# Kernel optimization log

Hardware: AMD Instinct MI355X
Metric: run time of the kernel (lower is better)

The kernel has to match this reference:

```python
import jax, jax.numpy as jnp
import numpy as np

N, E, F_IN, H, D, HID, G = 50000, 800000, 64, 4, 32, 128, 1024
NEG_SLOPE = 0.2


def setup_inputs():
    key = jax.random.key(0)
    ks = jax.random.split(key, 32)
    inp = {
        "x": jax.random.normal(ks[0], (N, F_IN), dtype=jnp.float32),
        "edge_index": jax.random.randint(ks[1], (2, E), 0, N, dtype=jnp.int64),
        "batch": jnp.sort(jax.random.randint(ks[2], (N,), 0, G, dtype=jnp.int64)),
    }
    dims = [F_IN, HID, HID]
    i = 3
    for l, din in enumerate(dims):
        s = 1.0 / np.sqrt(din)
        inp[f"Wl{l}"] = jax.random.normal(ks[i], (din, H * D), dtype=jnp.float32) * s; i += 1
        inp[f"bl{l}"] = jnp.zeros((H * D,), dtype=jnp.float32)
        inp[f"Wr{l}"] = jax.random.normal(ks[i], (din, H * D), dtype=jnp.float32) * s; i += 1
        inp[f"br{l}"] = jnp.zeros((H * D,), dtype=jnp.float32)
        inp[f"att{l}"] = jax.random.normal(ks[i], (H, D), dtype=jnp.float32) * (1.0 / np.sqrt(D)); i += 1
        inp[f"b{l}"] = jnp.zeros((H * D,), dtype=jnp.float32)
    inp["Wh"] = jax.random.normal(ks[i], (HID, 1), dtype=jnp.float32) * (1.0 / np.sqrt(HID))
    inp["bh"] = jnp.zeros((1,), dtype=jnp.float32)
    return inp


def gatv2_layer(x, src, dst, Wl, bl, Wr, br, att, b):
    # GATv2Conv (eval mode, no dropout): e_ij = att . leaky_relu(Wl x_j + Wr x_i)
    xl = (x @ Wl + bl).reshape(-1, H, D)   # source transform
    xr = (x @ Wr + br).reshape(-1, H, D)   # target transform
    m = xl[src] + xr[dst]                  # [E,H,D]
    e = jnp.where(m >= 0, m, NEG_SLOPE * m)
    score = jnp.einsum("ehd,hd->eh", e, att)          # [E,H]
    smax = jax.ops.segment_max(score, dst, num_segments=N)  # [N,H]
    expv = jnp.exp(score - smax[dst])
    denom = jax.ops.segment_sum(expv, dst, num_segments=N)
    alpha = expv / denom[dst]                          # softmax over in-edges of dst
    agg = jax.ops.segment_sum(alpha[:, :, None] * xl[src], dst, num_segments=N)
    return agg.reshape(-1, H * D) + b


def reference(x, edge_index, batch, Wl0, bl0, Wr0, br0, att0, b0,
              Wl1, bl1, Wr1, br1, att1, b1,
              Wl2, bl2, Wr2, br2, att2, b2, Wh, bh):
    src, dst = edge_index[0], edge_index[1]
    params = [(Wl0, bl0, Wr0, br0, att0, b0),
              (Wl1, bl1, Wr1, br1, att1, b1),
              (Wl2, bl2, Wr2, br2, att2, b2)]
    h = x
    for p in params:
        h = gatv2_layer(h, src, dst, *p)
        h = jax.nn.elu(h)  # dropout inactive in eval
    # global mean pool over graphs
    sums = jax.ops.segment_sum(h, batch, num_segments=G)
    cnt = jax.ops.segment_sum(jnp.ones((h.shape[0],), h.dtype), batch, num_segments=G)
    pooled = sums / jnp.maximum(cnt, 1.0)[:, None]
    return pooled @ Wh + bh
```

## Files before the change

kernel.cpp:

```cpp
#include <hip/hip_runtime.h>
#include <math.h>

#define N_NODES 50000
#define N_EDGES 800000
#define HD 128
#define GG 1024
#define NEG_SLOPE 0.2f
#define SCAN_B 1024
#define NB ((N_NODES + SCAN_B - 1) / SCAN_B)

typedef __attribute__((ext_vector_type(8))) short bf16x8;
typedef __attribute__((ext_vector_type(4))) float f32x4;

__device__ __forceinline__ unsigned short f2bf(float v) {
    unsigned u = __float_as_uint(v);
    u += 0x7fff + ((u >> 16) & 1);
    return (unsigned short)(u >> 16);
}
__device__ __forceinline__ float bf2f(unsigned short s) {
    return __uint_as_float((unsigned)s << 16);
}

__global__ void convert_x(const float* __restrict__ x, unsigned short* __restrict__ Xh,
                          unsigned short* __restrict__ Xl, int total)
{
    int i = blockIdx.x * 256 + threadIdx.x;
    if (i >= total) return;
    float v = x[i];
    unsigned short hi = f2bf(v);
    unsigned short lo = f2bf(v - bf2f(hi));
    Xh[i] = hi; Xl[i] = lo;
}

__global__ void convert_w(const float* __restrict__ Wl, const float* __restrict__ Wr,
                          unsigned short* __restrict__ Wth, unsigned short* __restrict__ Wtl,
                          int K)
{
    int t = blockIdx.x * 256 + threadIdx.x;
    if (t >= 256 * K) return;
    int c = t / K, k = t - c * K;
    float v = (c < 128) ? Wl[(size_t)k * 128 + c] : Wr[(size_t)k * 128 + (c - 128)];
    unsigned short hi = f2bf(v);
    unsigned short lo = f2bf(v - bf2f(hi));
    Wth[t] = hi; Wtl[t] = lo;
}

template<int K>
__launch_bounds__(256)
__global__ void gemm_mfma(const unsigned short* __restrict__ Xh, const unsigned short* __restrict__ Xl,
                          const unsigned short* __restrict__ Wth, const unsigned short* __restrict__ Wtl,
                          const float* __restrict__ bl, const float* __restrict__ br,
                          float* __restrict__ Cl, float* __restrict__ Cr, int n)
{
    constexpr int KC = 32;
    constexpr int NCH = K / KC;
    constexpr int XR = 40;
    __shared__ unsigned short XsH[64 * XR], XsL[64 * XR];
    __shared__ unsigned short WsH[256 * XR], WsL[256 * XR];
    const int tid  = threadIdx.x;
    const int wave = tid >> 6;
    const int lane = tid & 63;
    const int quad = lane >> 4;
    const int l15  = lane & 15;
    const int row0 = blockIdx.x * 64;

    f32x4 acc[4][4];
    #pragma unroll
    for (int i = 0; i < 4; i++)
        #pragma unroll
        for (int j = 0; j < 4; j++) acc[i][j] = (f32x4){0.f, 0.f, 0.f, 0.f};

    for (int ch = 0; ch < NCH; ch++) {
        const int k0 = ch * KC;
        {
            const int r = tid >> 2, seg = tid & 3;
            const int row = row0 + r;
            const size_t go = (size_t)row * K + k0 + seg * 8;
            uint4 vh = make_uint4(0, 0, 0, 0), vl = make_uint4(0, 0, 0, 0);
            if (row < n) { vh = *(const uint4*)(Xh + go); vl = *(const uint4*)(Xl + go); }
            *(uint4*)&XsH[r * XR + seg * 8] = vh;
            *(uint4*)&XsL[r * XR + seg * 8] = vl;
        }
        #pragma unroll
        for (int i = 0; i < 4; i++) {
            const int f = tid + i * 256;
            const int wr = f >> 2, seg = f & 3;
            const size_t go = (size_t)wr * K + k0 + seg * 8;
            *(uint4*)&WsH[wr * XR + seg * 8] = *(const uint4*)(Wth + go);
            *(uint4*)&WsL[wr * XR + seg * 8] = *(const uint4*)(Wtl + go);
        }
        __syncthreads();

        bf16x8 ah[4], al[4];
        #pragma unroll
        for (int mt = 0; mt < 4; mt++) {
            ah[mt] = *(const bf16x8*)&XsH[(mt * 16 + l15) * XR + quad * 8];
            al[mt] = *(const bf16x8*)&XsL[(mt * 16 + l15) * XR + quad * 8];
        }
        #pragma unroll
        for (int nt = 0; nt < 4; nt++) {
            const int wr = wave * 64 + nt * 16 + l15;
            const bf16x8 bh = *(const bf16x8*)&WsH[wr * XR + quad * 8];
            const bf16x8 bo = *(const bf16x8*)&WsL[wr * XR + quad * 8];
            #pragma unroll
            for (int mt = 0; mt < 4; mt++) {
                acc[mt][nt] = __builtin_amdgcn_mfma_f32_16x16x32_bf16(ah[mt], bh, acc[mt][nt], 0, 0, 0);
                acc[mt][nt] = __builtin_amdgcn_mfma_f32_16x16x32_bf16(ah[mt], bo, acc[mt][nt], 0, 0, 0);
                acc[mt][nt] = __builtin_amdgcn_mfma_f32_16x16x32_bf16(al[mt], bh, acc[mt][nt], 0, 0, 0);
            }
        }
        __syncthreads();
    }

    const bool isL = (wave < 2);
    const int colbase = (wave & 1) * 64;
    const float* bias = isL ? bl : br;
    float* C = isL ? Cl : Cr;
    #pragma unroll
    for (int nt = 0; nt < 4; nt++) {
        const float bv = bias[colbase + nt * 16 + l15];
        #pragma unroll
        for (int mt = 0; mt < 4; mt++) {
            #pragma unroll
            for (int r = 0; r < 4; r++) {
                const int row = row0 + mt * 16 + quad * 4 + r;
                if (row < n)
                    C[(size_t)row * 128 + colbase + nt * 16 + l15] = acc[mt][nt][r] + bv;
            }
        }
    }
}

__global__ void deg_hist(const int* __restrict__ dst, int* __restrict__ deg) {
    int e = blockIdx.x * 256 + threadIdx.x;
    if (e < N_EDGES) atomicAdd(&deg[dst[e]], 1);
}

__launch_bounds__(SCAN_B)
__global__ void scan_block(const int* __restrict__ deg, int* __restrict__ rowptr,
                           int* __restrict__ btot)
{
    __shared__ int s[SCAN_B];
    const int tid = threadIdx.x;
    const int i = blockIdx.x * SCAN_B + tid;
    int v = (i < N_NODES) ? deg[i] : 0;
    s[tid] = v;
    __syncthreads();
    for (int off = 1; off < SCAN_B; off <<= 1) {
        int t = (tid >= off) ? s[tid - off] : 0;
        __syncthreads();
        s[tid] += t;
        __syncthreads();
    }
    if (i < N_NODES) rowptr[i] = s[tid] - v;
    if (tid == SCAN_B - 1) btot[blockIdx.x] = s[SCAN_B - 1];
}

__global__ void scan_btot(const int* __restrict__ btot, int* __restrict__ boff) {
    if (threadIdx.x == 0) {
        int a = 0;
        for (int b = 0; b < NB; b++) { boff[b] = a; a += btot[b]; }
        boff[NB] = a;
    }
}

__global__ void scan_add(const int* __restrict__ boff, int* __restrict__ rowptr,
                         int* __restrict__ cursor)
{
    int i = blockIdx.x * 256 + threadIdx.x;
    if (i < N_NODES) {
        int r = rowptr[i] + boff[i >> 10];
        rowptr[i] = r;
        cursor[i] = r;
    }
    if (i == N_NODES) rowptr[N_NODES] = boff[NB];
}

__global__ void scatter_csr(const int* __restrict__ src, const int* __restrict__ dst,
                            int* __restrict__ cursor, int* __restrict__ csr_src)
{
    int e = blockIdx.x * 256 + threadIdx.x;
    if (e >= N_EDGES) return;
    int pos = atomicAdd(&cursor[dst[e]], 1);
    csr_src[pos] = src[e];
}

__global__ void build_gptr(const int* __restrict__ batch, int* __restrict__ gptr) {
    int i = blockIdx.x * 256 + threadIdx.x;
    if (i > N_NODES) return;
    if (i == 0) {
        for (int g = 0; g <= batch[0]; g++) gptr[g] = 0;
    } else if (i == N_NODES) {
        for (int g = batch[N_NODES - 1] + 1; g <= GG; g++) gptr[g] = N_NODES;
    } else {
        int b0 = batch[i - 1], b1 = batch[i];
        for (int g = b0 + 1; g <= b1; g++) gptr[g] = i;
    }
}

__launch_bounds__(256)
__global__ void node_attn(const float* __restrict__ xl, const float* __restrict__ xr,
                          const int* __restrict__ rowptr, const int* __restrict__ csr_src,
                          const float* __restrict__ att, const float* __restrict__ bvec,
                          unsigned short* __restrict__ Hh, unsigned short* __restrict__ Hl)
{
    const int node = (blockIdx.x * 256 + threadIdx.x) >> 6;
    const int lane = threadIdx.x & 63;
    if (node >= N_NODES) return;
    const int grp = lane >> 4;
    const int li  = lane & 15;

    const size_t nb = (size_t)node * HD + li * 8;
    const float4 xr0 = *(const float4*)(xr + nb);
    const float4 xr1 = *(const float4*)(xr + nb + 4);
    const float4 aw0 = *(const float4*)(att + li * 8);
    const float4 aw1 = *(const float4*)(att + li * 8 + 4);
    const int beg = rowptr[node];
    const int end = rowptr[node + 1];

    float m = -1e30f, l = 0.f;
    float4 a0 = make_float4(0.f, 0.f, 0.f, 0.f);
    float4 a1 = make_float4(0.f, 0.f, 0.f, 0.f);

    int e0 = beg + grp;
    int s0 = (e0 < end) ? csr_src[e0] : 0;
    float4 v0 = *(const float4*)(xl + (size_t)s0 * HD + li * 8);
    float4 v1 = *(const float4*)(xl + (size_t)s0 * HD + li * 8 + 4);

    for (int base = beg; base < end; base += 4) {
        const bool valid = (base + grp) < end;
        float4 n0 = v0, n1 = v1;
        if (base + 4 < end) {
            const int e2 = base + 4 + grp;
            const int s2 = (e2 < end) ? csr_src[e2] : 0;
            n0 = *(const float4*)(xl + (size_t)s2 * HD + li * 8);
            n1 = *(const float4*)(xl + (size_t)s2 * HD + li * 8 + 4);
        }
        float t, p;
        t = v0.x + xr0.x; t = fmaxf(t, NEG_SLOPE * t); p  = t * aw0.x;
        t = v0.y + xr0.y; t = fmaxf(t, NEG_SLOPE * t); p  = fmaf(t, aw0.y, p);
        t = v0.z + xr0.z; t = fmaxf(t, NEG_SLOPE * t); p  = fmaf(t, aw0.z, p);
        t = v0.w + xr0.w; t = fmaxf(t, NEG_SLOPE * t); p  = fmaf(t, aw0.w, p);
        t = v1.x + xr1.x; t = fmaxf(t, NEG_SLOPE * t); p  = fmaf(t, aw1.x, p);
        t = v1.y + xr1.y; t = fmaxf(t, NEG_SLOPE * t); p  = fmaf(t, aw1.y, p);
        t = v1.z + xr1.z; t = fmaxf(t, NEG_SLOPE * t); p  = fmaf(t, aw1.z, p);
        t = v1.w + xr1.w; t = fmaxf(t, NEG_SLOPE * t); p  = fmaf(t, aw1.w, p);
        p += __shfl_xor(p, 1);
        p += __shfl_xor(p, 2);

        const float mn = valid ? fmaxf(m, p) : m;
        const float w  = valid ? __expf(p - mn) : 0.f;
        const float sc = __expf(m - mn);
        l = fmaf(l, sc, w);
        a0.x = fmaf(a0.x, sc, w * v0.x);
        a0.y = fmaf(a0.y, sc, w * v0.y);
        a0.z = fmaf(a0.z, sc, w * v0.z);
        a0.w = fmaf(a0.w, sc, w * v0.w);
        a1.x = fmaf(a1.x, sc, w * v1.x);
        a1.y = fmaf(a1.y, sc, w * v1.y);
        a1.z = fmaf(a1.z, sc, w * v1.z);
        a1.w = fmaf(a1.w, sc, w * v1.w);
        m = mn;
        v0 = n0; v1 = n1;
    }

    #pragma unroll
    for (int off = 16; off < 64; off <<= 1) {
        const float mo = __shfl_xor(m, off);
        const float lo = __shfl_xor(l, off);
        float4 b0, b1;
        b0.x = __shfl_xor(a0.x, off); b0.y = __shfl_xor(a0.y, off);
        b0.z = __shfl_xor(a0.z, off); b0.w = __shfl_xor(a0.w, off);
        b1.x = __shfl_xor(a1.x, off); b1.y = __shfl_xor(a1.y, off);
        b1.z = __shfl_xor(a1.z, off); b1.w = __shfl_xor(a1.w, off);
        const float mm = fmaxf(m, mo);
        const float e1 = __expf(m - mm);
        const float e2 = __expf(mo - mm);
        l = l * e1 + lo * e2;
        a0.x = a0.x * e1 + b0.x * e2;
        a0.y = a0.y * e1 + b0.y * e2;
        a0.z = a0.z * e1 + b0.z * e2;
        a0.w = a0.w * e1 + b0.w * e2;
        a1.x = a1.x * e1 + b1.x * e2;
        a1.y = a1.y * e1 + b1.y * e2;
        a1.z = a1.z * e1 + b1.z * e2;
        a1.w = a1.w * e1 + b1.w * e2;
        m = mm;
    }

    if (grp == 0) {
        const float inv = (l > 0.f) ? 1.f / l : 0.f;
        const float4 bb0 = *(const float4*)(bvec + li * 8);
        const float4 bb1 = *(const float4*)(bvec + li * 8 + 4);
        float o[8];
        o[0] = fmaf(a0.x, inv, bb0.x);
        o[1] = fmaf(a0.y, inv, bb0.y);
        o[2] = fmaf(a0.z, inv, bb0.z);
        o[3] = fmaf(a0.w, inv, bb0.w);
        o[4] = fmaf(a1.x, inv, bb1.x);
        o[5] = fmaf(a1.y, inv, bb1.y);
        o[6] = fmaf(a1.z, inv, bb1.z);
        o[7] = fmaf(a1.w, inv, bb1.w);
        bf16x8 hv, lv;
        #pragma unroll
        for (int j = 0; j < 8; j++) {
            float e = (o[j] > 0.f) ? o[j] : expm1f(o[j]);
            unsigned short h = f2bf(e);
            hv[j] = (short)h;
            lv[j] = (short)f2bf(e - bf2f(h));
        }
        *(bf16x8*)(Hh + nb) = hv;
        *(bf16x8*)(Hl + nb) = lv;
    }
}

__launch_bounds__(256)
__global__ void pool_head(const unsigned short* __restrict__ Hh, const unsigned short* __restrict__ Hl,
                          const int* __restrict__ gptr, const float* __restrict__ Wh,
                          const float* __restrict__ bh, float* __restrict__ out)
{
    const int g = (blockIdx.x * 256 + threadIdx.x) >> 6;
    const int lane = threadIdx.x & 63;
    if (g >= GG) return;
    const int b0 = gptr[g], b1 = gptr[g + 1];
    const float2 w = *(const float2*)(Wh + lane * 2);
    float sx = 0.f, sy = 0.f;
    for (int i = b0; i < b1; i++) {
        const unsigned vh = *(const unsigned*)(Hh + (size_t)i * HD + lane * 2);
        const unsigned vl = *(const unsigned*)(Hl + (size_t)i * HD + lane * 2);
        sx += bf2f((unsigned short)(vh & 0xffff)) + bf2f((unsigned short)(vl & 0xffff));
        sy += bf2f((unsigned short)(vh >> 16))    + bf2f((unsigned short)(vl >> 16));
    }
    float d = sx * w.x + sy * w.y;
    d += __shfl_xor(d, 1);
    d += __shfl_xor(d, 2);
    d += __shfl_xor(d, 4);
    d += __shfl_xor(d, 8);
    d += __shfl_xor(d, 16);
    d += __shfl_xor(d, 32);
    if (lane == 0) out[g] = d / fmaxf((float)(b1 - b0), 1.f) + bh[0];
}

extern "C" void kernel_launch(void* const* d_in, const int* in_sizes, int n_in,
                              void* d_out, int out_size, void* d_ws, size_t ws_size,
                              hipStream_t stream)
{
    const float* x     = (const float*)d_in[0];
    const int*   edge  = (const int*)d_in[1];
    const int*   batch = (const int*)d_in[2];
    const int*   src   = edge;
    const int*   dst   = edge + N_EDGES;
    const float* Wh    = (const float*)d_in[21];
    const float* bh    = (const float*)d_in[22];
    float* out = (float*)d_out;

    const size_t N128 = (size_t)N_NODES * HD;
    float* buf_xl = (float*)d_ws;
    float* buf_xr = buf_xl + N128;
    unsigned short* Xh  = (unsigned short*)(buf_xr + N128);
    unsigned short* Xl_ = Xh + N128;
    unsigned short* Wth = Xl_ + N128;
    unsigned short* Wtl = Wth + 3 * 256 * 128;
    int* deg     = (int*)(Wtl + 3 * 256 * 128);
    int* rowptr  = deg + N_NODES;
    int* cursor  = rowptr + N_NODES + 1;
    int* csr_src = cursor + N_NODES;
    int* btot    = csr_src + N_EDGES;
    int* boff    = btot + NB;
    int* gptr    = boff + NB + 1;

    hipMemsetAsync(deg, 0, (size_t)N_NODES * sizeof(int), stream);
    deg_hist<<<(N_EDGES + 255) / 256, 256, 0, stream>>>(dst, deg);
    scan_block<<<NB, SCAN_B, 0, stream>>>(deg, rowptr, btot);
    scan_btot<<<1, 64, 0, stream>>>(btot, boff);
    scan_add<<<(N_NODES + 256) / 256, 256, 0, stream>>>(boff, rowptr, cursor);
    scatter_csr<<<(N_EDGES + 255) / 256, 256, 0, stream>>>(src, dst, cursor, csr_src);
    build_gptr<<<(N_NODES + 256) / 256, 256, 0, stream>>>(batch, gptr);

    convert_x<<<(N_NODES * 64 + 255) / 256, 256, 0, stream>>>(x, Xh, Xl_, N_NODES * 64);
    for (int l = 0; l < 3; l++) {
        const int K = (l == 0) ? 64 : 128;
        convert_w<<<(256 * K + 255) / 256, 256, 0, stream>>>(
            (const float*)d_in[3 + 6 * l], (const float*)d_in[5 + 6 * l],
            Wth + l * 256 * 128, Wtl + l * 256 * 128, K);
    }

    const int gemm_grid = (N_NODES + 63) / 64;
    const int attn_grid = (N_NODES + 3) / 4;

    for (int l = 0; l < 3; l++) {
        const float* bl  = (const float*)d_in[4 + 6 * l];
        const float* br  = (const float*)d_in[6 + 6 * l];
        const float* att = (const float*)d_in[7 + 6 * l];
        const float* bb  = (const float*)d_in[8 + 6 * l];

        if (l == 0)
            gemm_mfma<64><<<gemm_grid, 256, 0, stream>>>(Xh, Xl_, Wth, Wtl,
                                                         bl, br, buf_xl, buf_xr, N_NODES);
        else
            gemm_mfma<128><<<gemm_grid, 256, 0, stream>>>(Xh, Xl_,
                                                          Wth + l * 256 * 128, Wtl + l * 256 * 128,
                                                          bl, br, buf_xl, buf_xr, N_NODES);
        node_attn<<<attn_grid, 256, 0, stream>>>(buf_xl, buf_xr, rowptr, csr_src,
                                                 att, bb, Xh, Xl_);
    }

    pool_head<<<GG / 4, 256, 0, stream>>>(Xh, Xl_, gptr, Wh, bh, out);
}
```

Measured before the change: 516.2 us.

## Keep weights in registers with persistent GEMM waves and pack attention math

The GEMM becomes a persistent kernel. Each wave keeps a fixed 32-column slice of the split-bf16 weights in registers and walks over row tiles, reading X fragments straight from global memory, which removes the LDS staging and block barriers. Separately, the attention kernel's per-edge score and accumulation arithmetic is rewritten with packed v_pk_add/mul/fma f32 inline asm. The cost is that each X row is now read by 8 different waves instead of once per block, and the weight registers raise register pressure.

```diff
diff --git a/kernel.cpp b/kernel.cpp
--- a/kernel.cpp
+++ b/kernel.cpp
@@ -11,6 +11,7 @@
 
 typedef __attribute__((ext_vector_type(8))) short bf16x8;
 typedef __attribute__((ext_vector_type(4))) float f32x4;
+typedef __attribute__((ext_vector_type(2))) float f32x2;
 
 __device__ __forceinline__ unsigned short f2bf(float v) {
     unsigned u = __float_as_uint(v);
@@ -19,6 +20,16 @@
 }
 __device__ __forceinline__ float bf2f(unsigned short s) {
     return __uint_as_float((unsigned)s << 16);
+}
+
+__device__ __forceinline__ f32x2 pk_add(f32x2 a, f32x2 b) {
+    f32x2 d; asm("v_pk_add_f32 %0, %1, %2" : "=v"(d) : "v"(a), "v"(b)); return d;
+}
+__device__ __forceinline__ f32x2 pk_mul(f32x2 a, f32x2 b) {
+    f32x2 d; asm("v_pk_mul_f32 %0, %1, %2" : "=v"(d) : "v"(a), "v"(b)); return d;
+}
+__device__ __forceinline__ f32x2 pk_fma(f32x2 a, f32x2 b, f32x2 c) {
+    f32x2 d; asm("v_pk_fma_f32 %0, %1, %2, %3" : "=v"(d) : "v"(a), "v"(b), "v"(c)); return d;
 }
 
 __global__ void convert_x(const float* __restrict__ x, unsigned short* __restrict__ Xh,
@@ -47,87 +58,79 @@
 
 template<int K>
 __launch_bounds__(256)
-__global__ void gemm_mfma(const unsigned short* __restrict__ Xh, const unsigned short* __restrict__ Xl,
-                          const unsigned short* __restrict__ Wth, const unsigned short* __restrict__ Wtl,
-                          const float* __restrict__ bl, const float* __restrict__ br,
-                          float* __restrict__ Cl, float* __restrict__ Cr, int n)
-{
-    constexpr int KC = 32;
-    constexpr int NCH = K / KC;
-    constexpr int XR = 40;
-    __shared__ unsigned short XsH[64 * XR], XsL[64 * XR];
-    __shared__ unsigned short WsH[256 * XR], WsL[256 * XR];
+__global__ void gemm_reg(const unsigned short* __restrict__ Xh, const unsigned short* __restrict__ Xl,
+                         const unsigned short* __restrict__ Wth, const unsigned short* __restrict__ Wtl,
+                         const float* __restrict__ bl, const float* __restrict__ br,
+                         float* __restrict__ Cl, float* __restrict__ Cr, int n)
+{
+    constexpr int NCH = K / 32;
+    constexpr int RT  = (N_NODES + 63) / 64;
     const int tid  = threadIdx.x;
     const int wave = tid >> 6;
     const int lane = tid & 63;
     const int quad = lane >> 4;
     const int l15  = lane & 15;
-    const int row0 = blockIdx.x * 64;
-
-    f32x4 acc[4][4];
+    const int wid  = blockIdx.x * 4 + wave;
+    const int colid = wid & 7;
+    const int cb32  = colid * 32;
+    const int rs    = wid >> 3;
+    const int NS    = (gridDim.x * 4) >> 3;
+
+    bf16x8 Bh[NCH][2], Bo[NCH][2];
     #pragma unroll
-    for (int i = 0; i < 4; i++)
-        #pragma unroll
-        for (int j = 0; j < 4; j++) acc[i][j] = (f32x4){0.f, 0.f, 0.f, 0.f};
-
-    for (int ch = 0; ch < NCH; ch++) {
-        const int k0 = ch * KC;
-        {
-            const int r = tid >> 2, seg = tid & 3;
-            const int row = row0 + r;
-            const size_t go = (size_t)row * K + k0 + seg * 8;
-            uint4 vh = make_uint4(0, 0, 0, 0), vl = make_uint4(0, 0, 0, 0);
-            if (row < n) { vh = *(const uint4*)(Xh + go); vl = *(const uint4*)(Xl + go); }
-            *(uint4*)&XsH[r * XR + seg * 8] = vh;
-            *(uint4*)&XsL[r * XR + seg * 8] = vl;
-        }
-        #pragma unroll
-        for (int i = 0; i < 4; i++) {
-            const int f = tid + i * 256;
-            const int wr = f >> 2, seg = f & 3;
-            const size_t go = (size_t)wr * K + k0 + seg * 8;
-            *(uint4*)&WsH[wr * XR + seg * 8] = *(const uint4*)(Wth + go);
-            *(uint4*)&WsL[wr * XR + seg * 8] = *(const uint4*)(Wtl + go);
-        }
-        __syncthreads();
-
-        bf16x8 ah[4], al[4];
+    for (int ch = 0; ch < NCH; ch++)
+        #pragma unroll
+        for (int nt = 0; nt < 2; nt++) {
+            const size_t wo = (size_t)(cb32 + nt * 16 + l15) * K + ch * 32 + quad * 8;
+            Bh[ch][nt] = *(const bf16x8*)(Wth + wo);
+            Bo[ch][nt] = *(const bf16x8*)(Wtl + wo);
+        }
+
+    const int cb = cb32 & 127;
+    const float* bias = (colid < 4) ? bl : br;
+    float* C = (colid < 4) ? Cl : Cr;
+    float bv[2];
+    bv[0] = bias[cb + l15];
+    bv[1] = bias[cb + 16 + l15];
+
+    for (int rt = rs; rt < RT; rt += NS) {
+        const int row0 = rt * 64;
+        f32x4 acc[4][2];
         #pragma unroll
         for (int mt = 0; mt < 4; mt++) {
-            ah[mt] = *(const bf16x8*)&XsH[(mt * 16 + l15) * XR + quad * 8];
-            al[mt] = *(const bf16x8*)&XsL[(mt * 16 + l15) * XR + quad * 8];
-        }
-        #pragma unroll
-        for (int nt = 0; nt < 4; nt++) {
-            const int wr = wave * 64 + nt * 16 + l15;
-            const bf16x8 bh = *(const bf16x8*)&WsH[wr * XR + quad * 8];
-            const bf16x8 bo = *(const bf16x8*)&WsL[wr * XR + quad * 8];
+            acc[mt][0] = (f32x4){0.f, 0.f, 0.f, 0.f};
+            acc[mt][1] = (f32x4){0.f, 0.f, 0.f, 0.f};
+        }
+        #pragma unroll
+        for (int ch = 0; ch < NCH; ch++) {
+            bf16x8 ah[4], al[4];
             #pragma unroll
             for (int mt = 0; mt < 4; mt++) {
-                acc[mt][nt] = __builtin_amdgcn_mfma_f32_16x16x32_bf16(ah[mt], bh, acc[mt][nt], 0, 0, 0);
-                acc[mt][nt] = __builtin_amdgcn_mfma_f32_16x16x32_bf16(ah[mt], bo, acc[mt][nt], 0, 0, 0);
-                acc[mt][nt] = __builtin_amdgcn_mfma_f32_16x16x32_bf16(al[mt], bh, acc[mt][nt], 0, 0, 0);
+                int r = row0 + mt * 16 + l15;
+                r = (r < n) ? r : (n - 1);
+                const size_t go = (size_t)r * K + ch * 32 + quad * 8;
+                ah[mt] = *(const bf16x8*)(Xh + go);
+                al[mt] = *(const bf16x8*)(Xl + go);
             }
-        }
-        __syncthreads();
-    }
-
-    const bool isL = (wave < 2);
-    const int colbase = (wave & 1) * 64;
-    const float* bias = isL ? bl : br;
-    float* C = isL ? Cl : Cr;
-    #pragma unroll
-    for (int nt = 0; nt < 4; nt++) {
-        const float bv = bias[colbase + nt * 16 + l15];
-        #pragma unroll
-        for (int mt = 0; mt < 4; mt++) {
             #pragma unroll
-            for (int r = 0; r < 4; r++) {
-                const int row = row0 + mt * 16 + quad * 4 + r;
-                if (row < n)
-                    C[(size_t)row * 128 + colbase + nt * 16 + l15] = acc[mt][nt][r] + bv;
-            }
-        }
+            for (int nt = 0; nt < 2; nt++)
+                #pragma unroll
+                for (int mt = 0; mt < 4; mt++) {
+                    acc[mt][nt] = __builtin_amdgcn_mfma_f32_16x16x32_bf16(ah[mt], Bh[ch][nt], acc[mt][nt], 0, 0, 0);
+                    acc[mt][nt] = __builtin_amdgcn_mfma_f32_16x16x32_bf16(ah[mt], Bo[ch][nt], acc[mt][nt], 0, 0, 0);
+                    acc[mt][nt] = __builtin_amdgcn_mfma_f32_16x16x32_bf16(al[mt], Bh[ch][nt], acc[mt][nt], 0, 0, 0);
+                }
+        }
+        #pragma unroll
+        for (int nt = 0; nt < 2; nt++)
+            #pragma unroll
+            for (int mt = 0; mt < 4; mt++)
+                #pragma unroll
+                for (int r = 0; r < 4; r++) {
+                    const int row = row0 + mt * 16 + quad * 4 + r;
+                    if (row < n)
+                        C[(size_t)row * 128 + cb + nt * 16 + l15] = acc[mt][nt][r] + bv[nt];
+                }
     }
 }
 
@@ -211,40 +214,59 @@
     const int li  = lane & 15;
 
     const size_t nb = (size_t)node * HD + li * 8;
-    const float4 xr0 = *(const float4*)(xr + nb);
-    const float4 xr1 = *(const float4*)(xr + nb + 4);
-    const float4 aw0 = *(const float4*)(att + li * 8);
-    const float4 aw1 = *(const float4*)(att + li * 8 + 4);
+    f32x2 xrp[4], awp[4];
+    {
+        const float4 a = *(const float4*)(xr + nb);
+        const float4 b = *(const float4*)(xr + nb + 4);
+        xrp[0] = (f32x2){a.x, a.y}; xrp[1] = (f32x2){a.z, a.w};
+        xrp[2] = (f32x2){b.x, b.y}; xrp[3] = (f32x2){b.z, b.w};
+        const float4 c = *(const float4*)(att + li * 8);
+        const float4 d = *(const float4*)(att + li * 8 + 4);
+        awp[0] = (f32x2){c.x, c.y}; awp[1] = (f32x2){c.z, c.w};
+        awp[2] = (f32x2){d.x, d.y}; awp[3] = (f32x2){d.z, d.w};
+    }
+    const f32x2 nsl = (f32x2){NEG_SLOPE, NEG_SLOPE};
     const int beg = rowptr[node];
     const int end = rowptr[node + 1];
 
     float m = -1e30f, l = 0.f;
-    float4 a0 = make_float4(0.f, 0.f, 0.f, 0.f);
-    float4 a1 = make_float4(0.f, 0.f, 0.f, 0.f);
-
-    int e0 = beg + grp;
-    int s0 = (e0 < end) ? csr_src[e0] : 0;
-    float4 v0 = *(const float4*)(xl + (size_t)s0 * HD + li * 8);
-    float4 v1 = *(const float4*)(xl + (size_t)s0 * HD + li * 8 + 4);
+    f32x2 accp[4];
+    #pragma unroll
+    for (int j = 0; j < 4; j++) accp[j] = (f32x2){0.f, 0.f};
+
+    f32x2 vp[4];
+    {
+        const int e0 = beg + grp;
+        const int s0 = (e0 < end) ? csr_src[e0] : 0;
+        const float4 a = *(const float4*)(xl + (size_t)s0 * HD + li * 8);
+        const float4 b = *(const float4*)(xl + (size_t)s0 * HD + li * 8 + 4);
+        vp[0] = (f32x2){a.x, a.y}; vp[1] = (f32x2){a.z, a.w};
+        vp[2] = (f32x2){b.x, b.y}; vp[3] = (f32x2){b.z, b.w};
+    }
 
     for (int base = beg; base < end; base += 4) {
         const bool valid = (base + grp) < end;
-        float4 n0 = v0, n1 = v1;
+        f32x2 np[4];
+        #pragma unroll
+        for (int j = 0; j < 4; j++) np[j] = vp[j];
         if (base + 4 < end) {
             const int e2 = base + 4 + grp;
             const int s2 = (e2 < end) ? csr_src[e2] : 0;
-            n0 = *(const float4*)(xl + (size_t)s2 * HD + li * 8);
-            n1 = *(const float4*)(xl + (size_t)s2 * HD + li * 8 + 4);
-        }
-        float t, p;
-        t = v0.x + xr0.x; t = fmaxf(t, NEG_SLOPE * t); p  = t * aw0.x;
-        t = v0.y + xr0.y; t = fmaxf(t, NEG_SLOPE * t); p  = fmaf(t, aw0.y, p);
-        t = v0.z + xr0.z; t = fmaxf(t, NEG_SLOPE * t); p  = fmaf(t, aw0.z, p);
-        t = v0.w + xr0.w; t = fmaxf(t, NEG_SLOPE * t); p  = fmaf(t, aw0.w, p);
-        t = v1.x + xr1.x; t = fmaxf(t, NEG_SLOPE * t); p  = fmaf(t, aw1.x, p);
-        t = v1.y + xr1.y; t = fmaxf(t, NEG_SLOPE * t); p  = fmaf(t, aw1.y, p);
-        t = v1.z + xr1.z; t = fmaxf(t, NEG_SLOPE * t); p  = fmaf(t, aw1.z, p);
-        t = v1.w + xr1.w; t = fmaxf(t, NEG_SLOPE * t); p  = fmaf(t, aw1.w, p);
+            const float4 a = *(const float4*)(xl + (size_t)s2 * HD + li * 8);
+            const float4 b = *(const float4*)(xl + (size_t)s2 * HD + li * 8 + 4);
+            np[0] = (f32x2){a.x, a.y}; np[1] = (f32x2){a.z, a.w};
+            np[2] = (f32x2){b.x, b.y}; np[3] = (f32x2){b.z, b.w};
+        }
+        f32x2 pd = (f32x2){0.f, 0.f};
+        #pragma unroll
+        for (int j = 0; j < 4; j++) {
+            f32x2 t = pk_add(vp[j], xrp[j]);
+            f32x2 u = pk_mul(t, nsl);
+            t[0] = fmaxf(t[0], u[0]);
+            t[1] = fmaxf(t[1], u[1]);
+            pd = pk_fma(t, awp[j], pd);
+        }
+        float p = pd[0] + pd[1];
         p += __shfl_xor(p, 1);
         p += __shfl_xor(p, 2);
 
@@ -252,39 +274,35 @@
         const float w  = valid ? __expf(p - mn) : 0.f;
         const float sc = __expf(m - mn);
         l = fmaf(l, sc, w);
-        a0.x = fmaf(a0.x, sc, w * v0.x);
-        a0.y = fmaf(a0.y, sc, w * v0.y);
-        a0.z = fmaf(a0.z, sc, w * v0.z);
-        a0.w = fmaf(a0.w, sc, w * v0.w);
-        a1.x = fmaf(a1.x, sc, w * v1.x);
-        a1.y = fmaf(a1.y, sc, w * v1.y);
-        a1.z = fmaf(a1.z, sc, w * v1.z);
-        a1.w = fmaf(a1.w, sc, w * v1.w);
+        const f32x2 w2  = (f32x2){w, w};
+        const f32x2 sc2 = (f32x2){sc, sc};
+        #pragma unroll
+        for (int j = 0; j < 4; j++) {
+            accp[j] = pk_fma(accp[j], sc2, pk_mul(w2, vp[j]));
+            vp[j] = np[j];
+        }
         m = mn;
-        v0 = n0; v1 = n1;
     }
 
     #pragma unroll
     for (int off = 16; off < 64; off <<= 1) {
         const float mo = __shfl_xor(m, off);
         const float lo = __shfl_xor(l, off);
-        float4 b0, b1;
-        b0.x = __shfl_xor(a0.x, off); b0.y = __shfl_xor(a0.y, off);
-        b0.z = __shfl_xor(a0.z, off); b0.w = __shfl_xor(a0.w, off);
-        b1.x = __shfl_xor(a1.x, off); b1.y = __shfl_xor(a1.y, off);
-        b1.z = __shfl_xor(a1.z, off); b1.w = __shfl_xor(a1.w, off);
+        f32x2 bo[4];
+        #pragma unroll
+        for (int j = 0; j < 4; j++) {
+            bo[j][0] = __shfl_xor(accp[j][0], off);
+            bo[j][1] = __shfl_xor(accp[j][1], off);
+        }
         const float mm = fmaxf(m, mo);
         const float e1 = __expf(m - mm);
         const float e2 = __expf(mo - mm);
         l = l * e1 + lo * e2;
-        a0.x = a0.x * e1 + b0.x * e2;
-        a0.y = a0.y * e1 + b0.y * e2;
-        a0.z = a0.z * e1 + b0.z * e2;
-        a0.w = a0.w * e1 + b0.w * e2;
-        a1.x = a1.x * e1 + b1.x * e2;
-        a1.y = a1.y * e1 + b1.y * e2;
-        a1.z = a1.z * e1 + b1.z * e2;
-        a1.w = a1.w * e1 + b1.w * e2;
+        const f32x2 e1p = (f32x2){e1, e1};
+        const f32x2 e2p = (f32x2){e2, e2};
+        #pragma unroll
+        for (int j = 0; j < 4; j++)
+            accp[j] = pk_fma(accp[j], e1p, pk_mul(bo[j], e2p));
         m = mm;
     }
 
@@ -293,14 +311,14 @@
         const float4 bb0 = *(const float4*)(bvec + li * 8);
         const float4 bb1 = *(const float4*)(bvec + li * 8 + 4);
         float o[8];
-        o[0] = fmaf(a0.x, inv, bb0.x);
-        o[1] = fmaf(a0.y, inv, bb0.y);
-        o[2] = fmaf(a0.z, inv, bb0.z);
-        o[3] = fmaf(a0.w, inv, bb0.w);
-        o[4] = fmaf(a1.x, inv, bb1.x);
-        o[5] = fmaf(a1.y, inv, bb1.y);
-        o[6] = fmaf(a1.z, inv, bb1.z);
-        o[7] = fmaf(a1.w, inv, bb1.w);
+        o[0] = fmaf(accp[0][0], inv, bb0.x);
+        o[1] = fmaf(accp[0][1], inv, bb0.y);
+        o[2] = fmaf(accp[1][0], inv, bb0.z);
+        o[3] = fmaf(accp[1][1], inv, bb0.w);
+        o[4] = fmaf(accp[2][0], inv, bb1.x);
+        o[5] = fmaf(accp[2][1], inv, bb1.y);
+        o[6] = fmaf(accp[3][0], inv, bb1.z);
+        o[7] = fmaf(accp[3][1], inv, bb1.w);
         bf16x8 hv, lv;
         #pragma unroll
         for (int j = 0; j < 8; j++) {
@@ -385,7 +403,7 @@
             Wth + l * 256 * 128, Wtl + l * 256 * 128, K);
     }
 
-    const int gemm_grid = (N_NODES + 63) / 64;
+    const int gemm_grid = 522;
     const int attn_grid = (N_NODES + 3) / 4;
 
     for (int l = 0; l < 3; l++) {
@@ -395,12 +413,12 @@
         const float* bb  = (const float*)d_in[8 + 6 * l];
 
         if (l == 0)
-            gemm_mfma<64><<<gemm_grid, 256, 0, stream>>>(Xh, Xl_, Wth, Wtl,
+            gemm_reg<64><<<gemm_grid, 256, 0, stream>>>(Xh, Xl_, Wth, Wtl,
+                                                        bl, br, buf_xl, buf_xr, N_NODES);
+        else
+            gemm_reg<128><<<gemm_grid, 256, 0, stream>>>(Xh, Xl_,
+                                                         Wth + l * 256 * 128, Wtl + l * 256 * 128,
                                                          bl, br, buf_xl, buf_xr, N_NODES);
-        else
-            gemm_mfma<128><<<gemm_grid, 256, 0, stream>>>(Xh, Xl_,
-                                                          Wth + l * 256 * 128, Wtl + l * 256 * 128,
-                                                          bl, br, buf_xl, buf_xr, N_NODES);
         node_attn<<<attn_grid, 256, 0, stream>>>(buf_xl, buf_xr, rowptr, csr_src,
                                                  att, bb, Xh, Xl_);
     }
```

New measurement: 540.8 us. +4.8%, slower.
